# Performance work log

Hardware: AMD Instinct MI355X
Metric: run time of the kernel (lower is better)

The kernel has to match this reference:

```python
import jax, jax.numpy as jnp
import numpy as np

N_NODES = 50000
N_EDGES = 800000
N_GRAPHS = 256
IN_CH = 128
HID = 256
FFN = 256
OUT = 1


def xavier(key, shape):
    fan_in, fan_out = shape[0], shape[1]
    a = jnp.sqrt(6.0 / (fan_in + fan_out))
    return jax.random.uniform(key, shape, jnp.float32, -a, a)


def setup_inputs() -> dict:
    key = jax.random.key(0)
    ks = jax.random.split(key, 12)
    x = jax.random.normal(ks[0], (N_NODES, IN_CH), jnp.float32)
    edge_index = jax.random.randint(ks[1], (2, N_EDGES), 0, N_NODES, jnp.int32)
    batch = jnp.sort(jax.random.randint(ks[2], (N_NODES,), 0, N_GRAPHS, jnp.int32))
    return {
        "x": x,
        "edge_index": edge_index,
        "batch": batch,
        # GCNConv layers (glorot weight, zero bias as in PyG reset_parameters)
        "W1": xavier(ks[3], (IN_CH, HID)), "b1": jnp.zeros((HID,), jnp.float32),
        "W2": xavier(ks[4], (HID, HID)),   "b2": jnp.zeros((HID,), jnp.float32),
        "W3": xavier(ks[5], (HID, HID)),   "b3": jnp.zeros((HID,), jnp.float32),
        # FFN: Linear(HID, FFN) then final Linear(FFN, OUT)
        "Wf": xavier(ks[6], (HID, FFN)),   "bf": jnp.zeros((FFN,), jnp.float32),
        "Wo": xavier(ks[7], (FFN, OUT)),   "bo": jnp.zeros((OUT,), jnp.float32),
    }


def _gcn_norm(edge_index, n_nodes):
    # add self-loops, compute symmetric normalization D^-1/2 (A+I) D^-1/2
    loops = jnp.arange(n_nodes, dtype=edge_index.dtype)
    row = jnp.concatenate([edge_index[0], loops])
    col = jnp.concatenate([edge_index[1], loops])
    deg = jax.ops.segment_sum(jnp.ones_like(col, jnp.float32), col, num_segments=n_nodes)
    dis = jnp.where(deg > 0, jax.lax.rsqrt(jnp.maximum(deg, 1.0)), 0.0)
    norm = dis[row] * dis[col]  # [E+N]
    return row, col, norm


def _gcn_conv(x, W, b, row, col, norm, n_nodes):
    xw = x @ W                                   # [N, H]
    msg = xw[row] * norm[:, None]                # gather + scale  [E+N, H]
    out = jax.ops.segment_sum(msg, col, num_segments=n_nodes)
    return out + b


def reference(x, edge_index, batch, W1, b1, W2, b2, W3, b3, Wf, bf, Wo, bo):
    row, col, norm = _gcn_norm(edge_index, N_NODES)
    h = jax.nn.relu(_gcn_conv(x, W1, b1, row, col, norm, N_NODES))
    h = jax.nn.relu(_gcn_conv(h, W2, b2, row, col, norm, N_NODES))
    h = jax.nn.relu(_gcn_conv(h, W3, b3, row, col, norm, N_NODES))
    # global mean pool over graphs
    counts = jax.ops.segment_sum(jnp.ones((N_NODES,), jnp.float32), batch, num_segments=N_GRAPHS)
    pooled = jax.ops.segment_sum(h, batch, num_segments=N_GRAPHS) / jnp.maximum(counts, 1.0)[:, None]
    # FFN (dropout is identity in eval mode): Linear -> ReLU -> final Linear
    g = jax.nn.relu(pooled @ Wf + bf)
    out = g @ Wo + bo
    return out
```

## Files before the change

kernel.cpp:

```cpp
#include <hip/hip_runtime.h>
#include <hip/hip_bf16.h>
#include <hip/hip_fp16.h>


#define THREADS 256

typedef _Float16 f16x8 __attribute__((ext_vector_type(8)));
typedef float    f32x4 __attribute__((ext_vector_type(4)));


__global__ void degree_goff_kernel(const int* __restrict__ col, int* __restrict__ deg, int E,
                                   const int* __restrict__ batch, int* __restrict__ goff,
                                   int N, int G) {
    int i = blockIdx.x * THREADS + threadIdx.x;
    if (i < E) atomicAdd(&deg[col[i]], 1);
    if (i < N) {
        int b1 = batch[i];
        int b0 = (i == 0) ? -1 : batch[i - 1];
        for (int g = b0 + 1; g <= b1; ++g) goff[g] = i;
        if (i == N - 1) {
            for (int g = b1 + 1; g <= G; ++g) goff[g] = N;
        }
    }
}

__global__ __launch_bounds__(256) void scanA_kernel(
    const int* __restrict__ in, int* __restrict__ out, int* __restrict__ bsum,
    float* __restrict__ dis, int n) {
    __shared__ int wsum[4];
    int i0 = blockIdx.x * 1024 + threadIdx.x * 4;
    int lane = threadIdx.x & 63, wid = threadIdx.x >> 6;
    int v0 = 0, v1 = 0, v2 = 0, v3 = 0;
    if (i0 + 3 < n) {
        int4 v = *(const int4*)&in[i0];
        v0 = v.x; v1 = v.y; v2 = v.z; v3 = v.w;
    } else {
        if (i0 + 0 < n) v0 = in[i0 + 0];
        if (i0 + 1 < n) v1 = in[i0 + 1];
        if (i0 + 2 < n) v2 = in[i0 + 2];
        if (i0 + 3 < n) v3 = in[i0 + 3];
    }
    if (i0 + 0 < n) dis[i0 + 0] = rsqrtf((float)(v0 + 1));
    if (i0 + 1 < n) dis[i0 + 1] = rsqrtf((float)(v1 + 1));
    if (i0 + 2 < n) dis[i0 + 2] = rsqrtf((float)(v2 + 1));
    if (i0 + 3 < n) dis[i0 + 3] = rsqrtf((float)(v3 + 1));
    int s = v0 + v1 + v2 + v3;
    int inc = s;
    #pragma unroll
    for (int d = 1; d < 64; d <<= 1) {
        int t = __shfl_up(inc, d);
        if (lane >= d) inc += t;
    }
    if (lane == 63) wsum[wid] = inc;
    __syncthreads();
    int add = 0;
    for (int w = 0; w < wid; ++w) add += wsum[w];
    int ex = add + inc - s;
    if (i0 + 0 < n) out[i0 + 0] = ex;
    if (i0 + 1 < n) out[i0 + 1] = ex + v0;
    if (i0 + 2 < n) out[i0 + 2] = ex + v0 + v1;
    if (i0 + 3 < n) out[i0 + 3] = ex + v0 + v1 + v2;
    if (threadIdx.x == 255) bsum[blockIdx.x] = add + inc;
}

__global__ void scanB_kernel(int* __restrict__ bsum, int* __restrict__ total_slot, int nb) {
    int lane = threadIdx.x;
    int v = (lane < nb) ? bsum[lane] : 0;
    int inc = v;
    #pragma unroll
    for (int d = 1; d < 64; d <<= 1) {
        int t = __shfl_up(inc, d);
        if (lane >= d) inc += t;
    }
    if (lane < nb) bsum[lane] = inc - v;
    if (lane == 63) *total_slot = inc;
}

__global__ void scanC_kernel(int* __restrict__ out, const int* __restrict__ bsum, int n) {
    int i = blockIdx.x * THREADS + threadIdx.x;
    if (i < n) out[i] += bsum[i >> 10];
}

__global__ void csr_fill_kernel(const int* __restrict__ row, const int* __restrict__ col,
                                const int* __restrict__ offs, int* __restrict__ deg,
                                int* __restrict__ srcs, int E) {
    int e = blockIdx.x * THREADS + threadIdx.x;
    if (e < E) {
        int c = col[e];
        int old = atomicSub(&deg[c], 1);
        srcs[offs[c] + old - 1] = row[e];
    }
}

__global__ void xcvt_scale_kernel(const float* __restrict__ X, const float* __restrict__ dis,
                                  _Float16* __restrict__ Xs, int total8, int IC) {
    int i = blockIdx.x * THREADS + threadIdx.x;
    if (i >= total8) return;
    int idx = i * 8;
    float d = dis[idx / IC];
    float4 a = *(const float4*)&X[idx];
    float4 b = *(const float4*)&X[idx + 4];
    f16x8 o;
    o[0] = (_Float16)(d * a.x); o[1] = (_Float16)(d * a.y);
    o[2] = (_Float16)(d * a.z); o[3] = (_Float16)(d * a.w);
    o[4] = (_Float16)(d * b.x); o[5] = (_Float16)(d * b.y);
    o[6] = (_Float16)(d * b.z); o[7] = (_Float16)(d * b.w);
    *(f16x8*)&Xs[idx] = o;
}

__global__ void wcvt_kernel(const float* __restrict__ W, _Float16* __restrict__ T, int K, int Nc) {
    int i = blockIdx.x * THREADS + threadIdx.x;
    if (i >= K * Nc) return;
    int k = i / Nc, n = i % Nc;
    T[n * K + k] = (_Float16)W[i];
}


template<int LPN>
__global__ __launch_bounds__(256) void aggregate_f16_kernel(
    const _Float16* __restrict__ X, const int* __restrict__ offs,
    const int* __restrict__ srcs, const float* __restrict__ dis,
    _Float16* __restrict__ A, int N) {
    constexpr int NPB = 256 / LPN;
    int node = blockIdx.x * NPB + threadIdx.x / LPN;
    if (node >= N) return;
    int lane = threadIdx.x % LPN;
    const f16x8* Xv = (const f16x8*)X;
    f16x8 self = Xv[(size_t)node * LPN + lane];
    float acc[8], acc2[8];
    #pragma unroll
    for (int j = 0; j < 8; ++j) { acc[j] = (float)self[j]; acc2[j] = 0.f; }
    int s = offs[node], e = offs[node + 1];
    int i = s;
    for (; i + 4 <= e; i += 4) {
        int s0 = srcs[i], s1 = srcs[i + 1], s2 = srcs[i + 2], s3 = srcs[i + 3];
        f16x8 v0 = Xv[(size_t)s0 * LPN + lane];
        f16x8 v1 = Xv[(size_t)s1 * LPN + lane];
        f16x8 v2 = Xv[(size_t)s2 * LPN + lane];
        f16x8 v3 = Xv[(size_t)s3 * LPN + lane];
        #pragma unroll
        for (int j = 0; j < 8; ++j) {
            acc[j]  += (float)v0[j] + (float)v2[j];
            acc2[j] += (float)v1[j] + (float)v3[j];
        }
    }
    for (; i < e; ++i) {
        int s0 = srcs[i];
        f16x8 v0 = Xv[(size_t)s0 * LPN + lane];
        #pragma unroll
        for (int j = 0; j < 8; ++j) acc[j] += (float)v0[j];
    }
    float dn = dis[node];
    f16x8 o;
    #pragma unroll
    for (int j = 0; j < 8; ++j) o[j] = (_Float16)(dn * (acc[j] + acc2[j]));
    ((f16x8*)A)[(size_t)node * LPN + lane] = o;
}


template<int K, bool SCALE>
__global__ __launch_bounds__(256) void gemm_f16_kernel(
    const _Float16* __restrict__ A, const _Float16* __restrict__ B,
    const float* __restrict__ bias, const float* __restrict__ dscale,
    _Float16* __restrict__ H, int M) {
    constexpr int BM = 128, BN = 128, LST = 40;
    __shared__ _Float16 As[BM * LST];
    __shared__ _Float16 Bs[BN * LST];
    int tid = threadIdx.x;
    int m0 = blockIdx.y * BM, n0 = blockIdx.x * BN;
    int wid = tid >> 6, lane = tid & 63;
    int wm = (wid & 1) * 64, wn = (wid >> 1) * 64;
    int l16 = lane & 15, quad = lane >> 4;

    f32x4 acc[4][4] = {};

    for (int k0 = 0; k0 < K; k0 += 32) {
        #pragma unroll
        for (int rep = 0; rep < 2; ++rep) {
            int idx = tid + rep * 256;
            int r = idx >> 2, seg = idx & 3;
            int gr = m0 + r;
            uint4 va = make_uint4(0, 0, 0, 0);
            if (gr < M) va = *(const uint4*)&A[(size_t)gr * K + k0 + seg * 8];
            *(uint4*)&As[r * LST + seg * 8] = va;
            uint4 vb = *(const uint4*)&B[(size_t)(n0 + r) * K + k0 + seg * 8];
            *(uint4*)&Bs[r * LST + seg * 8] = vb;
        }
        __syncthreads();
        f16x8 bh[4];
        #pragma unroll
        for (int ni = 0; ni < 4; ++ni) {
            int n = wn + ni * 16 + l16;
            bh[ni] = *(const f16x8*)&Bs[n * LST + quad * 8];
        }
        #pragma unroll
        for (int mi = 0; mi < 4; ++mi) {
            int m = wm + mi * 16 + l16;
            f16x8 ah = *(const f16x8*)&As[m * LST + quad * 8];
            #pragma unroll
            for (int ni = 0; ni < 4; ++ni) {
                acc[mi][ni] = __builtin_amdgcn_mfma_f32_16x16x32_f16(ah, bh[ni], acc[mi][ni], 0, 0, 0);
            }
        }
        __syncthreads();
    }
    #pragma unroll
    for (int mi = 0; mi < 4; ++mi) {
        #pragma unroll
        for (int ni = 0; ni < 4; ++ni) {
            int col = n0 + wn + ni * 16 + l16;
            float bv = bias[col];
            #pragma unroll
            for (int r = 0; r < 4; ++r) {
                int grow = m0 + wm + mi * 16 + quad * 4 + r;
                if (grow < M) {
                    float v = fmaxf(acc[mi][ni][r] + bv, 0.f);
                    if (SCALE) v *= dscale[grow];
                    H[(size_t)grow * 256 + col] = (_Float16)v;
                }
            }
        }
    }
}


__global__ __launch_bounds__(256) void pool_part_kernel(
    const _Float16* __restrict__ H, const int* __restrict__ batch,
    float* __restrict__ pooled, int N) {
    __shared__ int bsh[64];
    int n0 = blockIdx.x * 64;
    if (threadIdx.x < 64) {
        int n = n0 + threadIdx.x;
        bsh[threadIdx.x] = (n < N) ? batch[n] : -1;
    }
    __syncthreads();
    int c = threadIdx.x;
    int lim = min(64, N - n0);
    if (lim <= 0) return;
    float acc = 0.f;
    int gcur = bsh[0];
    for (int j = 0; j < lim; ++j) {
        int g = bsh[j];
        if (g != gcur) {
            atomicAdd(&pooled[gcur * 256 + c], acc);
            acc = 0.f; gcur = g;
        }
        acc += (float)H[(size_t)(n0 + j) * 256 + c];
    }
    atomicAdd(&pooled[gcur * 256 + c], acc);
}


__global__ __launch_bounds__(256) void ffn_kernel(
    const float* __restrict__ pooled, const int* __restrict__ goff,
    const float* __restrict__ Wf, const float* __restrict__ bf,
    const float* __restrict__ Wo, const float* __restrict__ bo,
    float* __restrict__ out) {
    __shared__ float p[256];
    __shared__ float red[256];
    int g = blockIdx.x, t = threadIdx.x;
    int cnt = goff[g + 1] - goff[g];
    float inv = 1.f / (float)max(cnt, 1);
    p[t] = pooled[g * 256 + t] * inv;
    __syncthreads();
    float s = bf[t];
    #pragma unroll 8
    for (int k = 0; k < 256; ++k) s = fmaf(p[k], Wf[k * 256 + t], s);
    float gv = fmaxf(s, 0.f);
    red[t] = gv * Wo[t];
    __syncthreads();
    for (int o = 128; o > 0; o >>= 1) {
        if (t < o) red[t] += red[t + o];
        __syncthreads();
    }
    if (t == 0) out[g] = red[0] + bo[0];
}


extern "C" void kernel_launch(void* const* d_in, const int* in_sizes, int n_in,
                              void* d_out, int out_size, void* d_ws, size_t ws_size,
                              hipStream_t stream) {
    const float* x   = (const float*)d_in[0];
    const int*   ei  = (const int*)d_in[1];
    const int*   bat = (const int*)d_in[2];
    const float* W1  = (const float*)d_in[3];
    const float* b1  = (const float*)d_in[4];
    const float* W2  = (const float*)d_in[5];
    const float* b2  = (const float*)d_in[6];
    const float* W3  = (const float*)d_in[7];
    const float* b3  = (const float*)d_in[8];
    const float* Wf  = (const float*)d_in[9];
    const float* bf  = (const float*)d_in[10];
    const float* Wo  = (const float*)d_in[11];
    const float* bo  = (const float*)d_in[12];
    float* out = (float*)d_out;

    const int N  = in_sizes[2];
    const int E  = in_sizes[1] / 2;
    const int IC = in_sizes[0] / N;
    const int HID = 256;
    const int G  = out_size;
    const int* row = ei;
    const int* col = ei + E;

    char* w = (char*)d_ws;
    size_t off = 0;
    auto alloc = [&](size_t bytes) -> void* {
        void* p = w + off;
        off += (bytes + 255) & ~(size_t)255;
        return p;
    };
    int*   deg    = (int*)alloc((size_t)N * 4);
    float* dis    = (float*)alloc((size_t)N * 4);
    int*   offs   = (int*)alloc((size_t)(N + 1) * 4);
    int*   srcs   = (int*)alloc((size_t)E * 4);
    int*   goff   = (int*)alloc((size_t)(G + 1) * 4);
    int*   bsum   = (int*)alloc((size_t)64 * 4);
    _Float16* W1t = (_Float16*)alloc((size_t)HID * IC * 2);
    _Float16* W2t = (_Float16*)alloc((size_t)HID * HID * 2);
    _Float16* W3t = (_Float16*)alloc((size_t)HID * HID * 2);
    _Float16* Xs  = (_Float16*)alloc((size_t)N * IC * 2);
    _Float16* Ah  = (_Float16*)alloc((size_t)N * HID * 2);
    _Float16* Hs  = (_Float16*)alloc((size_t)N * HID * 2);
    float* pooled = (float*)alloc((size_t)G * HID * 4);
    (void)ws_size; (void)n_in;

    hipMemsetAsync(deg, 0, (size_t)N * 4, stream);
    hipMemsetAsync(pooled, 0, (size_t)G * HID * 4, stream);

    int nb = (N + 1023) / 1024;
    degree_goff_kernel<<<(E + THREADS - 1) / THREADS, THREADS, 0, stream>>>(
        col, deg, E, bat, goff, N, G);
    scanA_kernel<<<nb, 256, 0, stream>>>(deg, offs, bsum, dis, N);
    scanB_kernel<<<1, 64, 0, stream>>>(bsum, &offs[N], nb);
    scanC_kernel<<<(N + THREADS - 1) / THREADS, THREADS, 0, stream>>>(offs, bsum, N);
    csr_fill_kernel<<<(E + THREADS - 1) / THREADS, THREADS, 0, stream>>>(row, col, offs, deg, srcs, E);

    int total8 = N * IC / 8;
    xcvt_scale_kernel<<<(total8 + THREADS - 1) / THREADS, THREADS, 0, stream>>>(x, dis, Xs, total8, IC);
    wcvt_kernel<<<(IC * HID + THREADS - 1) / THREADS, THREADS, 0, stream>>>(W1, W1t, IC, HID);
    wcvt_kernel<<<(HID * HID + THREADS - 1) / THREADS, THREADS, 0, stream>>>(W2, W2t, HID, HID);
    wcvt_kernel<<<(HID * HID + THREADS - 1) / THREADS, THREADS, 0, stream>>>(W3, W3t, HID, HID);

    dim3 ggrid(HID / 128, (N + 127) / 128);
    aggregate_f16_kernel<16><<<(N + 15) / 16, 256, 0, stream>>>(Xs, offs, srcs, dis, Ah, N);
    gemm_f16_kernel<128, true><<<ggrid, 256, 0, stream>>>(Ah, W1t, b1, dis, Hs, N);
    aggregate_f16_kernel<32><<<(N + 7) / 8, 256, 0, stream>>>(Hs, offs, srcs, dis, Ah, N);
    gemm_f16_kernel<256, true><<<ggrid, 256, 0, stream>>>(Ah, W2t, b2, dis, Hs, N);
    aggregate_f16_kernel<32><<<(N + 7) / 8, 256, 0, stream>>>(Hs, offs, srcs, dis, Ah, N);
    gemm_f16_kernel<256, false><<<ggrid, 256, 0, stream>>>(Ah, W3t, b3, nullptr, Hs, N);

    pool_part_kernel<<<(N + 63) / 64, 256, 0, stream>>>(Hs, bat, pooled, N);
    ffn_kernel<<<G, 256, 0, stream>>>(pooled, goff, Wf, bf, Wo, bo, out);
}
```

Measured before the change: 459.8 us.

## Fuse neighbor aggregation into GEMM per 64-node tile and merge conversion kernels

```diff
diff --git a/kernel.cpp b/kernel.cpp
--- a/kernel.cpp
+++ b/kernel.cpp
@@ -92,111 +92,128 @@
     }
 }
 
-__global__ void xcvt_scale_kernel(const float* __restrict__ X, const float* __restrict__ dis,
-                                  _Float16* __restrict__ Xs, int total8, int IC) {
+__global__ void convert_kernel(
+    const float* __restrict__ X, const float* __restrict__ dis,
+    _Float16* __restrict__ Xs, int total8, int IC,
+    const float* __restrict__ W1, _Float16* __restrict__ W1t, int k1,
+    const float* __restrict__ W2, _Float16* __restrict__ W2t,
+    const float* __restrict__ W3, _Float16* __restrict__ W3t) {
     int i = blockIdx.x * THREADS + threadIdx.x;
-    if (i >= total8) return;
-    int idx = i * 8;
-    float d = dis[idx / IC];
-    float4 a = *(const float4*)&X[idx];
-    float4 b = *(const float4*)&X[idx + 4];
-    f16x8 o;
-    o[0] = (_Float16)(d * a.x); o[1] = (_Float16)(d * a.y);
-    o[2] = (_Float16)(d * a.z); o[3] = (_Float16)(d * a.w);
-    o[4] = (_Float16)(d * b.x); o[5] = (_Float16)(d * b.y);
-    o[6] = (_Float16)(d * b.z); o[7] = (_Float16)(d * b.w);
-    *(f16x8*)&Xs[idx] = o;
-}
-
-__global__ void wcvt_kernel(const float* __restrict__ W, _Float16* __restrict__ T, int K, int Nc) {
-    int i = blockIdx.x * THREADS + threadIdx.x;
-    if (i >= K * Nc) return;
-    int k = i / Nc, n = i % Nc;
-    T[n * K + k] = (_Float16)W[i];
-}
-
-
-template<int LPN>
-__global__ __launch_bounds__(256) void aggregate_f16_kernel(
+    if (i < total8) {
+        int idx = i * 8;
+        float d = dis[idx / IC];
+        float4 a = *(const float4*)&X[idx];
+        float4 b = *(const float4*)&X[idx + 4];
+        f16x8 o;
+        o[0] = (_Float16)(d * a.x); o[1] = (_Float16)(d * a.y);
+        o[2] = (_Float16)(d * a.z); o[3] = (_Float16)(d * a.w);
+        o[4] = (_Float16)(d * b.x); o[5] = (_Float16)(d * b.y);
+        o[6] = (_Float16)(d * b.z); o[7] = (_Float16)(d * b.w);
+        *(f16x8*)&Xs[idx] = o;
+        return;
+    }
+    int j = i - total8;
+    int n1 = k1 * 256;
+    if (j < n1) {
+        int k = j >> 8, n = j & 255;
+        W1t[n * k1 + k] = (_Float16)W1[j];
+        return;
+    }
+    j -= n1;
+    if (j < 65536) {
+        int k = j >> 8, n = j & 255;
+        W2t[n * 256 + k] = (_Float16)W2[j];
+        return;
+    }
+    j -= 65536;
+    if (j < 65536) {
+        int k = j >> 8, n = j & 255;
+        W3t[n * 256 + k] = (_Float16)W3[j];
+    }
+}
+
+
+template<int K, bool SCALE>
+__global__ __launch_bounds__(256, 3) void fused_layer_kernel(
     const _Float16* __restrict__ X, const int* __restrict__ offs,
     const int* __restrict__ srcs, const float* __restrict__ dis,
-    _Float16* __restrict__ A, int N) {
-    constexpr int NPB = 256 / LPN;
-    int node = blockIdx.x * NPB + threadIdx.x / LPN;
-    if (node >= N) return;
-    int lane = threadIdx.x % LPN;
-    const f16x8* Xv = (const f16x8*)X;
-    f16x8 self = Xv[(size_t)node * LPN + lane];
-    float acc[8], acc2[8];
-    #pragma unroll
-    for (int j = 0; j < 8; ++j) { acc[j] = (float)self[j]; acc2[j] = 0.f; }
-    int s = offs[node], e = offs[node + 1];
-    int i = s;
-    for (; i + 4 <= e; i += 4) {
-        int s0 = srcs[i], s1 = srcs[i + 1], s2 = srcs[i + 2], s3 = srcs[i + 3];
-        f16x8 v0 = Xv[(size_t)s0 * LPN + lane];
-        f16x8 v1 = Xv[(size_t)s1 * LPN + lane];
-        f16x8 v2 = Xv[(size_t)s2 * LPN + lane];
-        f16x8 v3 = Xv[(size_t)s3 * LPN + lane];
-        #pragma unroll
-        for (int j = 0; j < 8; ++j) {
-            acc[j]  += (float)v0[j] + (float)v2[j];
-            acc2[j] += (float)v1[j] + (float)v3[j];
-        }
-    }
-    for (; i < e; ++i) {
-        int s0 = srcs[i];
-        f16x8 v0 = Xv[(size_t)s0 * LPN + lane];
-        #pragma unroll
-        for (int j = 0; j < 8; ++j) acc[j] += (float)v0[j];
-    }
-    float dn = dis[node];
-    f16x8 o;
-    #pragma unroll
-    for (int j = 0; j < 8; ++j) o[j] = (_Float16)(dn * (acc[j] + acc2[j]));
-    ((f16x8*)A)[(size_t)node * LPN + lane] = o;
-}
-
-
-template<int K, bool SCALE>
-__global__ __launch_bounds__(256) void gemm_f16_kernel(
-    const _Float16* __restrict__ A, const _Float16* __restrict__ B,
-    const float* __restrict__ bias, const float* __restrict__ dscale,
-    _Float16* __restrict__ H, int M) {
-    constexpr int BM = 128, BN = 128, LST = 40;
-    __shared__ _Float16 As[BM * LST];
-    __shared__ _Float16 Bs[BN * LST];
+    const _Float16* __restrict__ Bt, const float* __restrict__ bias,
+    const float* __restrict__ dscale, _Float16* __restrict__ H, int N) {
+    constexpr int LSA = K + 8;
+    constexpr int LSB = 36;
+    __shared__ _Float16 As[64 * LSA];
+    __shared__ _Float16 Bs[256 * LSB];
     int tid = threadIdx.x;
-    int m0 = blockIdx.y * BM, n0 = blockIdx.x * BN;
+    int n0 = blockIdx.x * 64;
+
+    {
+        constexpr int LPN = K / 8;
+        constexpr int NPB = 256 / LPN;
+        int grp = tid / LPN, lane = tid % LPN;
+        const f16x8* Xv = (const f16x8*)X;
+        #pragma unroll
+        for (int pass = 0; pass < 64 / NPB; ++pass) {
+            int local = pass * NPB + grp;
+            int node = n0 + local;
+            float acc[8], acc2[8];
+            #pragma unroll
+            for (int j = 0; j < 8; ++j) { acc[j] = 0.f; acc2[j] = 0.f; }
+            float dn = 0.f;
+            if (node < N) {
+                dn = dis[node];
+                f16x8 self = Xv[(size_t)node * LPN + lane];
+                #pragma unroll
+                for (int j = 0; j < 8; ++j) acc[j] = (float)self[j];
+                int s = offs[node], e = offs[node + 1];
+                int i = s;
+                for (; i + 4 <= e; i += 4) {
+                    int s0 = srcs[i], s1 = srcs[i + 1], s2 = srcs[i + 2], s3 = srcs[i + 3];
+                    f16x8 v0 = Xv[(size_t)s0 * LPN + lane];
+                    f16x8 v1 = Xv[(size_t)s1 * LPN + lane];
+                    f16x8 v2 = Xv[(size_t)s2 * LPN + lane];
+                    f16x8 v3 = Xv[(size_t)s3 * LPN + lane];
+                    #pragma unroll
+                    for (int j = 0; j < 8; ++j) {
+                        acc[j]  += (float)v0[j] + (float)v2[j];
+                        acc2[j] += (float)v1[j] + (float)v3[j];
+                    }
+                }
+                for (; i < e; ++i) {
+                    int s0 = srcs[i];
+                    f16x8 v0 = Xv[(size_t)s0 * LPN + lane];
+                    #pragma unroll
+                    for (int j = 0; j < 8; ++j) acc[j] += (float)v0[j];
+                }
+            }
+            f16x8 o;
+            #pragma unroll
+            for (int j = 0; j < 8; ++j) o[j] = (_Float16)(dn * (acc[j] + acc2[j]));
+            *(f16x8*)&As[local * LSA + lane * 8] = o;
+        }
+    }
+    __syncthreads();
+
     int wid = tid >> 6, lane = tid & 63;
-    int wm = (wid & 1) * 64, wn = (wid >> 1) * 64;
     int l16 = lane & 15, quad = lane >> 4;
-
+    int wn = wid * 64;
     f32x4 acc[4][4] = {};
 
     for (int k0 = 0; k0 < K; k0 += 32) {
         #pragma unroll
-        for (int rep = 0; rep < 2; ++rep) {
-            int idx = tid + rep * 256;
+        for (int rep = 0; rep < 4; ++rep) {
+            int idx = rep * 256 + tid;
             int r = idx >> 2, seg = idx & 3;
-            int gr = m0 + r;
-            uint4 va = make_uint4(0, 0, 0, 0);
-            if (gr < M) va = *(const uint4*)&A[(size_t)gr * K + k0 + seg * 8];
-            *(uint4*)&As[r * LST + seg * 8] = va;
-            uint4 vb = *(const uint4*)&B[(size_t)(n0 + r) * K + k0 + seg * 8];
-            *(uint4*)&Bs[r * LST + seg * 8] = vb;
+            *(uint4*)&Bs[r * LSB + seg * 8] = *(const uint4*)&Bt[(size_t)r * K + k0 + seg * 8];
         }
         __syncthreads();
         f16x8 bh[4];
         #pragma unroll
         for (int ni = 0; ni < 4; ++ni) {
-            int n = wn + ni * 16 + l16;
-            bh[ni] = *(const f16x8*)&Bs[n * LST + quad * 8];
+            bh[ni] = *(const f16x8*)&Bs[(wn + ni * 16 + l16) * LSB + quad * 8];
         }
         #pragma unroll
         for (int mi = 0; mi < 4; ++mi) {
-            int m = wm + mi * 16 + l16;
-            f16x8 ah = *(const f16x8*)&As[m * LST + quad * 8];
+            f16x8 ah = *(const f16x8*)&As[(mi * 16 + l16) * LSA + k0 + quad * 8];
             #pragma unroll
             for (int ni = 0; ni < 4; ++ni) {
                 acc[mi][ni] = __builtin_amdgcn_mfma_f32_16x16x32_f16(ah, bh[ni], acc[mi][ni], 0, 0, 0);
@@ -204,16 +221,17 @@
         }
         __syncthreads();
     }
+
     #pragma unroll
     for (int mi = 0; mi < 4; ++mi) {
         #pragma unroll
         for (int ni = 0; ni < 4; ++ni) {
-            int col = n0 + wn + ni * 16 + l16;
+            int col = wn + ni * 16 + l16;
             float bv = bias[col];
             #pragma unroll
             for (int r = 0; r < 4; ++r) {
-                int grow = m0 + wm + mi * 16 + quad * 4 + r;
-                if (grow < M) {
+                int grow = n0 + mi * 16 + quad * 4 + r;
+                if (grow < N) {
                     float v = fmaxf(acc[mi][ni][r] + bv, 0.f);
                     if (SCALE) v *= dscale[grow];
                     H[(size_t)grow * 256 + col] = (_Float16)v;
@@ -320,8 +338,8 @@
     _Float16* W2t = (_Float16*)alloc((size_t)HID * HID * 2);
     _Float16* W3t = (_Float16*)alloc((size_t)HID * HID * 2);
     _Float16* Xs  = (_Float16*)alloc((size_t)N * IC * 2);
-    _Float16* Ah  = (_Float16*)alloc((size_t)N * HID * 2);
     _Float16* Hs  = (_Float16*)alloc((size_t)N * HID * 2);
+    _Float16* Hs2 = (_Float16*)alloc((size_t)N * HID * 2);
     float* pooled = (float*)alloc((size_t)G * HID * 4);
     (void)ws_size; (void)n_in;
 
@@ -337,18 +355,17 @@
     csr_fill_kernel<<<(E + THREADS - 1) / THREADS, THREADS, 0, stream>>>(row, col, offs, deg, srcs, E);
 
     int total8 = N * IC / 8;
-    xcvt_scale_kernel<<<(total8 + THREADS - 1) / THREADS, THREADS, 0, stream>>>(x, dis, Xs, total8, IC);
-    wcvt_kernel<<<(IC * HID + THREADS - 1) / THREADS, THREADS, 0, stream>>>(W1, W1t, IC, HID);
-    wcvt_kernel<<<(HID * HID + THREADS - 1) / THREADS, THREADS, 0, stream>>>(W2, W2t, HID, HID);
-    wcvt_kernel<<<(HID * HID + THREADS - 1) / THREADS, THREADS, 0, stream>>>(W3, W3t, HID, HID);
-
-    dim3 ggrid(HID / 128, (N + 127) / 128);
-    aggregate_f16_kernel<16><<<(N + 15) / 16, 256, 0, stream>>>(Xs, offs, srcs, dis, Ah, N);
-    gemm_f16_kernel<128, true><<<ggrid, 256, 0, stream>>>(Ah, W1t, b1, dis, Hs, N);
-    aggregate_f16_kernel<32><<<(N + 7) / 8, 256, 0, stream>>>(Hs, offs, srcs, dis, Ah, N);
-    gemm_f16_kernel<256, true><<<ggrid, 256, 0, stream>>>(Ah, W2t, b2, dis, Hs, N);
-    aggregate_f16_kernel<32><<<(N + 7) / 8, 256, 0, stream>>>(Hs, offs, srcs, dis, Ah, N);
-    gemm_f16_kernel<256, false><<<ggrid, 256, 0, stream>>>(Ah, W3t, b3, nullptr, Hs, N);
+    int conv_total = total8 + IC * HID + HID * HID + HID * HID;
+    convert_kernel<<<(conv_total + THREADS - 1) / THREADS, THREADS, 0, stream>>>(
+        x, dis, Xs, total8, IC, W1, W1t, IC, W2, W2t, W3, W3t);
+
+    int ntiles = (N + 63) / 64;
+    fused_layer_kernel<128, true><<<ntiles, 256, 0, stream>>>(
+        Xs, offs, srcs, dis, W1t, b1, dis, Hs, N);
+    fused_layer_kernel<256, true><<<ntiles, 256, 0, stream>>>(
+        Hs, offs, srcs, dis, W2t, b2, dis, Hs2, N);
+    fused_layer_kernel<256, false><<<ntiles, 256, 0, stream>>>(
+        Hs2, offs, srcs, dis, W3t, b3, nullptr, Hs, N);
 
     pool_part_kernel<<<(N + 63) / 64, 256, 0, stream>>>(Hs, bat, pooled, N);
     ffn_kernel<<<G, 256, 0, stream>>>(pooled, goff, Wf, bf, Wo, bo, out);
```

Result: slower. 497.0 us (+8.1%).

## Fuse mean-pool into last GEMM epilogue and merge conversion kernels

Applied to the files above, without the earlier changes.

```diff
diff --git a/kernel.cpp b/kernel.cpp
--- a/kernel.cpp
+++ b/kernel.cpp
@@ -92,27 +92,44 @@
     }
 }
 
-__global__ void xcvt_scale_kernel(const float* __restrict__ X, const float* __restrict__ dis,
-                                  _Float16* __restrict__ Xs, int total8, int IC) {
+__global__ void convert_kernel(
+    const float* __restrict__ X, const float* __restrict__ dis,
+    _Float16* __restrict__ Xs, int total8, int IC,
+    const float* __restrict__ W1, _Float16* __restrict__ W1t, int k1,
+    const float* __restrict__ W2, _Float16* __restrict__ W2t,
+    const float* __restrict__ W3, _Float16* __restrict__ W3t) {
     int i = blockIdx.x * THREADS + threadIdx.x;
-    if (i >= total8) return;
-    int idx = i * 8;
-    float d = dis[idx / IC];
-    float4 a = *(const float4*)&X[idx];
-    float4 b = *(const float4*)&X[idx + 4];
-    f16x8 o;
-    o[0] = (_Float16)(d * a.x); o[1] = (_Float16)(d * a.y);
-    o[2] = (_Float16)(d * a.z); o[3] = (_Float16)(d * a.w);
-    o[4] = (_Float16)(d * b.x); o[5] = (_Float16)(d * b.y);
-    o[6] = (_Float16)(d * b.z); o[7] = (_Float16)(d * b.w);
-    *(f16x8*)&Xs[idx] = o;
-}
-
-__global__ void wcvt_kernel(const float* __restrict__ W, _Float16* __restrict__ T, int K, int Nc) {
-    int i = blockIdx.x * THREADS + threadIdx.x;
-    if (i >= K * Nc) return;
-    int k = i / Nc, n = i % Nc;
-    T[n * K + k] = (_Float16)W[i];
+    if (i < total8) {
+        int idx = i * 8;
+        float d = dis[idx / IC];
+        float4 a = *(const float4*)&X[idx];
+        float4 b = *(const float4*)&X[idx + 4];
+        f16x8 o;
+        o[0] = (_Float16)(d * a.x); o[1] = (_Float16)(d * a.y);
+        o[2] = (_Float16)(d * a.z); o[3] = (_Float16)(d * a.w);
+        o[4] = (_Float16)(d * b.x); o[5] = (_Float16)(d * b.y);
+        o[6] = (_Float16)(d * b.z); o[7] = (_Float16)(d * b.w);
+        *(f16x8*)&Xs[idx] = o;
+        return;
+    }
+    int j = i - total8;
+    int n1 = k1 * 256;
+    if (j < n1) {
+        int k = j >> 8, n = j & 255;
+        W1t[n * k1 + k] = (_Float16)W1[j];
+        return;
+    }
+    j -= n1;
+    if (j < 65536) {
+        int k = j >> 8, n = j & 255;
+        W2t[n * 256 + k] = (_Float16)W2[j];
+        return;
+    }
+    j -= 65536;
+    if (j < 65536) {
+        int k = j >> 8, n = j & 255;
+        W3t[n * 256 + k] = (_Float16)W3[j];
+    }
 }
 
 
@@ -158,22 +175,29 @@
 }
 
 
-template<int K, bool SCALE>
+template<int K, int MODE>
 __global__ __launch_bounds__(256) void gemm_f16_kernel(
     const _Float16* __restrict__ A, const _Float16* __restrict__ B,
     const float* __restrict__ bias, const float* __restrict__ dscale,
-    _Float16* __restrict__ H, int M) {
+    _Float16* __restrict__ H, float* __restrict__ pooled,
+    const int* __restrict__ batch, int M) {
     constexpr int BM = 128, BN = 128, LST = 40;
     __shared__ _Float16 As[BM * LST];
     __shared__ _Float16 Bs[BN * LST];
+    __shared__ int bsh[BM];
     int tid = threadIdx.x;
     int m0 = blockIdx.y * BM, n0 = blockIdx.x * BN;
     int wid = tid >> 6, lane = tid & 63;
     int wm = (wid & 1) * 64, wn = (wid >> 1) * 64;
     int l16 = lane & 15, quad = lane >> 4;
 
+    if (MODE == 2) {
+        if (tid < BM) bsh[tid] = batch[min(m0 + tid, M - 1)];
+    }
+
     f32x4 acc[4][4] = {};
 
+    #pragma unroll
     for (int k0 = 0; k0 < K; k0 += 32) {
         #pragma unroll
         for (int rep = 0; rep < 2; ++rep) {
@@ -204,50 +228,51 @@
         }
         __syncthreads();
     }
+
     #pragma unroll
     for (int mi = 0; mi < 4; ++mi) {
+        int base_local = wm + mi * 16;
+        int g0 = 0, g15 = 0;
+        if (MODE == 2) { g0 = bsh[base_local]; g15 = bsh[base_local + 15]; }
         #pragma unroll
         for (int ni = 0; ni < 4; ++ni) {
             int col = n0 + wn + ni * 16 + l16;
             float bv = bias[col];
-            #pragma unroll
-            for (int r = 0; r < 4; ++r) {
-                int grow = m0 + wm + mi * 16 + quad * 4 + r;
-                if (grow < M) {
-                    float v = fmaxf(acc[mi][ni][r] + bv, 0.f);
-                    if (SCALE) v *= dscale[grow];
-                    H[(size_t)grow * 256 + col] = (_Float16)v;
+            if (MODE == 1) {
+                #pragma unroll
+                for (int r = 0; r < 4; ++r) {
+                    int grow = m0 + base_local + quad * 4 + r;
+                    if (grow < M) {
+                        float v = fmaxf(acc[mi][ni][r] + bv, 0.f) * dscale[grow];
+                        H[(size_t)grow * 256 + col] = (_Float16)v;
+                    }
+                }
+            } else {
+                if (g0 == g15) {
+                    float p = 0.f;
+                    #pragma unroll
+                    for (int r = 0; r < 4; ++r) {
+                        int grow = m0 + base_local + quad * 4 + r;
+                        float v = fmaxf(acc[mi][ni][r] + bv, 0.f);
+                        p += (grow < M) ? v : 0.f;
+                    }
+                    p += __shfl_xor(p, 16);
+                    p += __shfl_xor(p, 32);
+                    if (quad == 0) atomicAdd(&pooled[g0 * 256 + col], p);
+                } else {
+                    #pragma unroll
+                    for (int r = 0; r < 4; ++r) {
+                        int local = base_local + quad * 4 + r;
+                        int grow = m0 + local;
+                        if (grow < M) {
+                            float v = fmaxf(acc[mi][ni][r] + bv, 0.f);
+                            atomicAdd(&pooled[bsh[local] * 256 + col], v);
+                        }
+                    }
                 }
             }
         }
     }
-}
-
-
-__global__ __launch_bounds__(256) void pool_part_kernel(
-    const _Float16* __restrict__ H, const int* __restrict__ batch,
-    float* __restrict__ pooled, int N) {
-    __shared__ int bsh[64];
-    int n0 = blockIdx.x * 64;
-    if (threadIdx.x < 64) {
-        int n = n0 + threadIdx.x;
-        bsh[threadIdx.x] = (n < N) ? batch[n] : -1;
-    }
-    __syncthreads();
-    int c = threadIdx.x;
-    int lim = min(64, N - n0);
-    if (lim <= 0) return;
-    float acc = 0.f;
-    int gcur = bsh[0];
-    for (int j = 0; j < lim; ++j) {
-        int g = bsh[j];
-        if (g != gcur) {
-            atomicAdd(&pooled[gcur * 256 + c], acc);
-            acc = 0.f; gcur = g;
-        }
-        acc += (float)H[(size_t)(n0 + j) * 256 + c];
-    }
-    atomicAdd(&pooled[gcur * 256 + c], acc);
 }
 
 
@@ -337,19 +362,17 @@
     csr_fill_kernel<<<(E + THREADS - 1) / THREADS, THREADS, 0, stream>>>(row, col, offs, deg, srcs, E);
 
     int total8 = N * IC / 8;
-    xcvt_scale_kernel<<<(total8 + THREADS - 1) / THREADS, THREADS, 0, stream>>>(x, dis, Xs, total8, IC);
-    wcvt_kernel<<<(IC * HID + THREADS - 1) / THREADS, THREADS, 0, stream>>>(W1, W1t, IC, HID);
-    wcvt_kernel<<<(HID * HID + THREADS - 1) / THREADS, THREADS, 0, stream>>>(W2, W2t, HID, HID);
-    wcvt_kernel<<<(HID * HID + THREADS - 1) / THREADS, THREADS, 0, stream>>>(W3, W3t, HID, HID);
+    int conv_total = total8 + IC * HID + HID * HID + HID * HID;
+    convert_kernel<<<(conv_total + THREADS - 1) / THREADS, THREADS, 0, stream>>>(
+        x, dis, Xs, total8, IC, W1, W1t, IC, W2, W2t, W3, W3t);
 
     dim3 ggrid(HID / 128, (N + 127) / 128);
     aggregate_f16_kernel<16><<<(N + 15) / 16, 256, 0, stream>>>(Xs, offs, srcs, dis, Ah, N);
-    gemm_f16_kernel<128, true><<<ggrid, 256, 0, stream>>>(Ah, W1t, b1, dis, Hs, N);
+    gemm_f16_kernel<128, 1><<<ggrid, 256, 0, stream>>>(Ah, W1t, b1, dis, Hs, nullptr, nullptr, N);
     aggregate_f16_kernel<32><<<(N + 7) / 8, 256, 0, stream>>>(Hs, offs, srcs, dis, Ah, N);
-    gemm_f16_kernel<256, true><<<ggrid, 256, 0, stream>>>(Ah, W2t, b2, dis, Hs, N);
+    gemm_f16_kernel<256, 1><<<ggrid, 256, 0, stream>>>(Ah, W2t, b2, dis, Hs, nullptr, nullptr, N);
     aggregate_f16_kernel<32><<<(N + 7) / 8, 256, 0, stream>>>(Hs, offs, srcs, dis, Ah, N);
-    gemm_f16_kernel<256, false><<<ggrid, 256, 0, stream>>>(Ah, W3t, b3, nullptr, Hs, N);
-
-    pool_part_kernel<<<(N + 63) / 64, 256, 0, stream>>>(Hs, bat, pooled, N);
+    gemm_f16_kernel<256, 2><<<ggrid, 256, 0, stream>>>(Ah, W3t, b3, nullptr, nullptr, pooled, bat, N);
+
     ffn_kernel<<<G, 256, 0, stream>>>(pooled, goff, Wf, bf, Wo, bo, out);
 }
```

Result: faster. 448.4 us (-2.5%).
